# Kernel tuning notes

Hardware: AMD Instinct MI355X
Metric: run time of the kernel (lower is better)

Reference implementation:

```python
import jax, jax.numpy as jnp
import numpy as np

N_NODES = 50000
N_EDGES = 800000
IN_FEAT = 256
OUT_FEAT = 256
NUM_RELS = 64
NUM_BASES = 8


def setup_inputs() -> dict:
    key = jax.random.key(0)
    ks = jax.random.split(key, 9)
    x = jax.random.normal(ks[0], (N_NODES, IN_FEAT), dtype=jnp.float32)
    src = jax.random.randint(ks[1], (N_EDGES,), 0, N_NODES, dtype=jnp.int32)
    dst = jax.random.randint(ks[2], (N_EDGES,), 0, N_NODES, dtype=jnp.int32)
    etypes = jax.random.randint(ks[3], (N_EDGES,), 0, NUM_RELS, dtype=jnp.int32)
    norm = jax.random.uniform(ks[4], (N_EDGES, 1), dtype=jnp.float32)
    # glorot-style params
    s_w = (6.0 / (IN_FEAT + OUT_FEAT)) ** 0.5
    weight = jax.random.uniform(ks[5], (NUM_BASES, IN_FEAT, OUT_FEAT), jnp.float32, -s_w, s_w)
    s_c = (6.0 / (NUM_RELS + NUM_BASES)) ** 0.5
    w_comp = jax.random.uniform(ks[6], (NUM_RELS, NUM_BASES), jnp.float32, -s_c, s_c)
    h_bias = jnp.zeros((OUT_FEAT,), jnp.float32)
    loop_weight = jax.random.uniform(ks[7], (IN_FEAT, OUT_FEAT), jnp.float32, -s_w, s_w)
    return {"x": x, "src": src, "dst": dst, "etypes": etypes, "norm": norm,
            "weight": weight, "w_comp": w_comp, "h_bias": h_bias,
            "loop_weight": loop_weight}


def reference(x, src, dst, etypes, norm, weight, w_comp, h_bias, loop_weight):
    # Basis regularizer with num_bases < num_rels:
    #   W_r = sum_b w_comp[r, b] * V_b
    # Per-edge message: msg_e = (x[src_e] @ W_{etype_e}) * norm_e,
    # aggregated by sum onto destination nodes. Since the map is linear,
    # we aggregate per basis first, then apply V_b (8 dense GEMMs).
    n_nodes = x.shape[0]
    coef = w_comp[etypes]                      # [E, B] per-edge basis coeffs
    xs = x[src] * norm                         # [E, D] normalized source feats
    out = jnp.zeros((n_nodes, weight.shape[2]), x.dtype)
    for b in range(weight.shape[0]):           # small fixed loop over bases
        agg = jax.ops.segment_sum(xs * coef[:, b:b + 1], dst,
                                  num_segments=n_nodes)   # [N, D]
        out = out + agg @ weight[b]            # [N, O]
    out = out + h_bias + x @ loop_weight       # bias + self-loop
    return jax.nn.relu(out)
```

## Files before the change

### kernel.cpp

```cpp
#include <hip/hip_runtime.h>
#include <hip/hip_bf16.h>
#include <stdint.h>

#define N_NODES 50000
#define N_EDGES 800000
#define IN_FEAT 256
#define OUT_FEAT 256
#define NUM_RELS 64
#define NUM_BASES 8
#define KTOT 2304
#define KAGG 2048
#define MP 50176
#define NT 36
#define SCAN_BLKS 196

typedef __attribute__((ext_vector_type(8))) __bf16 bf16x8;
typedef __attribute__((ext_vector_type(4))) __bf16 bf16x4;
typedef __attribute__((ext_vector_type(4))) float f32x4;
typedef __attribute__((ext_vector_type(2))) float f32x2;

static __device__ __forceinline__ void gload_lds16(const void* g, void* l) {
  auto gp = (const __attribute__((address_space(1))) void*)(uintptr_t)g;
  auto lp = (__attribute__((address_space(3))) void*)(uint32_t)(uintptr_t)l;
  __builtin_amdgcn_global_load_lds(gp, lp, 16, 0, 0);
}

__global__ void k_prex(const float* __restrict__ x, __bf16* __restrict__ xb) {
  int i = blockIdx.x * 256 + threadIdx.x;
  const float4* xp = (const float4*)x;
  float4 u = xp[i * 2], v = xp[i * 2 + 1];
  bf16x8 o;
  o[0] = (__bf16)u.x; o[1] = (__bf16)u.y; o[2] = (__bf16)u.z; o[3] = (__bf16)u.w;
  o[4] = (__bf16)v.x; o[5] = (__bf16)v.y; o[6] = (__bf16)v.z; o[7] = (__bf16)v.w;
  *(bf16x8*)(xb + (size_t)i * 8) = o;
}

__global__ void k_count(const int* __restrict__ dst, int* __restrict__ deg) {
  int e = blockIdx.x * 256 + threadIdx.x;
  atomicAdd(&deg[dst[e]], 1);
}

__global__ void k_scan1(const int* __restrict__ deg, int* __restrict__ offs,
                        int* __restrict__ bsum) {
  __shared__ int s[256];
  int t = threadIdx.x;
  int i = blockIdx.x * 256 + t;
  int v = (i < N_NODES) ? deg[i] : 0;
  s[t] = v;
  __syncthreads();
  for (int d = 1; d < 256; d <<= 1) {
    int y = (t >= d) ? s[t - d] : 0;
    __syncthreads();
    s[t] += y;
    __syncthreads();
  }
  if (i < N_NODES) offs[i] = s[t] - v;
  if (t == 255) bsum[blockIdx.x] = s[255];
}

__global__ void k_scan3(int* __restrict__ offs, const int* __restrict__ bsum,
                        int* __restrict__ fill) {
  __shared__ int s[256];
  int t = threadIdx.x;
  s[t] = (t < SCAN_BLKS && t < blockIdx.x) ? bsum[t] : 0;
  __syncthreads();
  for (int d = 128; d; d >>= 1) {
    if (t < d) s[t] += s[t + d];
    __syncthreads();
  }
  int base = s[0];
  int i = blockIdx.x * 256 + t;
  if (i < N_NODES) {
    int o = offs[i] + base;
    offs[i] = o;
    fill[i] = o;
  }
}

__global__ void k_scatter(const int* __restrict__ dst, const int* __restrict__ srcv,
                          const int* __restrict__ ety, const float* __restrict__ norm,
                          int* __restrict__ fill, uint2* __restrict__ erec) {
  int e = blockIdx.x * 256 + threadIdx.x;
  int pos = atomicAdd(&fill[dst[e]], 1);
  erec[pos] = make_uint2((unsigned)srcv[e] | ((unsigned)ety[e] << 16),
                         __float_as_uint(norm[e]));
}

#define AGG_BODY(RX, RY, XV)                                                  \
  do {                                                                        \
    int et_ = (RX) >> 16;                                                     \
    float nm_ = __uint_as_float(RY);                                          \
    f32x2 v0_ = {__uint_as_float((XV).x << 16) * nm_,                         \
                 __uint_as_float((XV).x & 0xffff0000u) * nm_};                 \
    f32x2 v1_ = {__uint_as_float((XV).y << 16) * nm_,                         \
                 __uint_as_float((XV).y & 0xffff0000u) * nm_};                 \
    f32x4 cl_ = *(const f32x4*)&wc[et_ * 8];                                  \
    f32x4 ch_ = *(const f32x4*)&wc[et_ * 8 + 4];                              \
    _Pragma("unroll") for (int b = 0; b < 4; ++b) {                           \
      acc[b][0] += v0_ * cl_[b];                                              \
      acc[b][1] += v1_ * cl_[b];                                              \
      acc[b + 4][0] += v0_ * ch_[b];                                          \
      acc[b + 4][1] += v1_ * ch_[b];                                          \
    }                                                                         \
  } while (0)

__global__ __launch_bounds__(256) void k_agg(
    const __bf16* __restrict__ xb, const float* __restrict__ w_comp,
    const int* __restrict__ offs, const int* __restrict__ fin,
    const uint2* __restrict__ erec, __bf16* __restrict__ A) {
  __shared__ float wc[NUM_RELS * NUM_BASES];
  int t = threadIdx.x;
  wc[t] = w_comp[t];
  wc[t + 256] = w_comp[t + 256];
  __syncthreads();

  int wid = t >> 6, lane = t & 63;
  int node = blockIdx.x * 4 + wid;

  f32x2 acc[NUM_BASES][2];
#pragma unroll
  for (int b = 0; b < NUM_BASES; ++b) {
    acc[b][0] = f32x2{0.f, 0.f};
    acc[b][1] = f32x2{0.f, 0.f};
  }

  int i0 = offs[node];
  int cnt = fin[node] - i0;
  const uint2* rp = erec + i0;
  int lo4 = lane * 4;

  int i = 0;
  for (; i + 8 <= cnt; i += 8) {
    uint2 r[8];
#pragma unroll
    for (int j = 0; j < 8; ++j) r[j] = rp[i + j];
    uint2 xv[8];
#pragma unroll
    for (int j = 0; j < 8; ++j)
      xv[j] = *(const uint2*)(xb + (size_t)(r[j].x & 0xffff) * IN_FEAT + lo4);
#pragma unroll
    for (int j = 0; j < 8; ++j) AGG_BODY(r[j].x, r[j].y, xv[j]);
  }
  for (; i + 4 <= cnt; i += 4) {
    uint2 r[4];
#pragma unroll
    for (int j = 0; j < 4; ++j) r[j] = rp[i + j];
    uint2 xv[4];
#pragma unroll
    for (int j = 0; j < 4; ++j)
      xv[j] = *(const uint2*)(xb + (size_t)(r[j].x & 0xffff) * IN_FEAT + lo4);
#pragma unroll
    for (int j = 0; j < 4; ++j) AGG_BODY(r[j].x, r[j].y, xv[j]);
  }
  for (; i < cnt; ++i) {
    uint2 r = rp[i];
    uint2 xv = *(const uint2*)(xb + (size_t)(r.x & 0xffff) * IN_FEAT + lo4);
    AGG_BODY(r.x, r.y, xv);
  }

  __bf16* Ar = A + (size_t)node * KAGG + lo4;
#pragma unroll
  for (int b = 0; b < NUM_BASES; ++b) {
    bf16x4 o;
    o[0] = (__bf16)acc[b][0][0];
    o[1] = (__bf16)acc[b][0][1];
    o[2] = (__bf16)acc[b][1][0];
    o[3] = (__bf16)acc[b][1][1];
    *(bf16x4*)(Ar + b * 256) = o;
  }
}

__global__ void k_prepw(const float* __restrict__ weight, const float* __restrict__ loop_w,
                        __bf16* __restrict__ Wt) {
  int o = blockIdx.x;
  int t = threadIdx.x;
#pragma unroll
  for (int c = 0; c < 9; ++c) {
    int r = c * 256 + t;
    float v = (r < 2048) ? weight[(size_t)r * 256 + o]
                         : loop_w[(size_t)(r - 2048) * 256 + o];
    Wt[(size_t)o * KTOT + r] = (__bf16)v;
  }
}

__global__ __launch_bounds__(512, 1) void k_gemm(const __bf16* __restrict__ A,
                                                 const __bf16* __restrict__ xb,
                                                 const __bf16* __restrict__ Wt,
                                                 const float* __restrict__ bias,
                                                 float* __restrict__ out) {
  __shared__ __align__(16) __bf16 sA[2 * 256 * 64];
  __shared__ __align__(16) __bf16 sB[2 * 256 * 64];

  int t = threadIdx.x;
  int wid = t >> 6, lane = t & 63;
  int tm = blockIdx.x;
  int wr = wid >> 2;
  int wcol = wid & 3;
  int rfw = __builtin_amdgcn_readfirstlane(wid);

  f32x4 acc[8][4];
#pragma unroll
  for (int m = 0; m < 8; ++m)
#pragma unroll
    for (int n = 0; n < 4; ++n) acc[m][n] = f32x4{0.f, 0.f, 0.f, 0.f};

  int frow = lane & 15;
  int g = lane >> 4;
  int f7 = frow & 7;
  int kb0 = ((g ^ f7) << 4);
  int kb1 = (((4 + g) ^ f7) << 4);

  int rh = t >> 3;
  int qoff = ((t & 7) ^ (rh & 7)) * 8;
  const __bf16* gA[2][2];
  const __bf16* gX[2][2];
  const __bf16* gB[2][2];
#pragma unroll
  for (int h = 0; h < 2; ++h)
#pragma unroll
    for (int it = 0; it < 2; ++it) {
      int row = h * 128 + it * 64 + rh;
      gA[h][it] = A + (size_t)(tm * 256 + row) * KAGG + qoff;
      gX[h][it] = xb + (size_t)(tm * 256 + row) * IN_FEAT + qoff;
      gB[h][it] = Wt + (size_t)row * KTOT + qoff;
    }

  bf16x8 af[4][2];
  bf16x8 bh0[2][2], bh1[2][2];

#define VMWAIT(N) asm volatile("s_waitcnt vmcnt(" #N ")" ::: "memory")
#define BAR()                                       \
  do {                                              \
    asm volatile("" ::: "memory");                  \
    __builtin_amdgcn_s_barrier();                   \
    asm volatile("" ::: "memory");                  \
  } while (0)
#define PRIO(N) __builtin_amdgcn_s_setprio(N)

#define STAGE_A(H, U, BUF)                                                    \
  do {                                                                        \
    char* d_ = (char*)sA + (BUF) * 32768 + (H) * 16384 + rfw * 1024;          \
    if ((U) < 32) {                                                           \
      int ko_ = (U) * 64;                                                     \
      gload_lds16(gA[H][0] + ko_, d_);                                        \
      gload_lds16(gA[H][1] + ko_, d_ + 8192);                                 \
    } else {                                                                  \
      int ko_ = ((U) - 32) * 64;                                              \
      gload_lds16(gX[H][0] + ko_, d_);                                        \
      gload_lds16(gX[H][1] + ko_, d_ + 8192);                                 \
    }                                                                         \
  } while (0)

#define STAGE_B(H, U, BUF)                                                    \
  do {                                                                        \
    char* d_ = (char*)sB + (BUF) * 32768 + (H) * 16384 + rfw * 1024;          \
    int ko_ = (U) * 64;                                                       \
    gload_lds16(gB[H][0] + ko_, d_);                                          \
    gload_lds16(gB[H][1] + ko_, d_ + 8192);                                   \
  } while (0)

#define READ_A(BUF, MS)                                                       \
  do {                                                                        \
    const char* b_ = (const char*)sA + (BUF) * 32768;                         \
    _Pragma("unroll") for (int mf = 0; mf < 4; ++mf) {                        \
      int r_ = wr * 128 + (MS) * 64 + mf * 16 + frow;                         \
      af[mf][0] = *(const bf16x8*)(b_ + r_ * 128 + kb0);                      \
      af[mf][1] = *(const bf16x8*)(b_ + r_ * 128 + kb1);                      \
    }                                                                         \
  } while (0)

#define READ_B(BUF, NH, DST)                                                  \
  do {                                                                        \
    const char* b_ = (const char*)sB + (BUF) * 32768;                         \
    _Pragma("unroll") for (int nf = 0; nf < 2; ++nf) {                        \
      int r_ = wcol * 64 + ((NH) * 2 + nf) * 16 + frow;                       \
      DST[nf][0] = *(const bf16x8*)(b_ + r_ * 128 + kb0);                     \
      DST[nf][1] = *(const bf16x8*)(b_ + r_ * 128 + kb1);                     \
    }                                                                         \
  } while (0)

#define MFMA16(MS, NH, BS)                                                    \
  do {                                                                        \
    _Pragma("unroll") for (int mf = 0; mf < 4; ++mf)                          \
    _Pragma("unroll") for (int nf = 0; nf < 2; ++nf) {                        \
      acc[(MS) * 4 + mf][(NH) * 2 + nf] =                                     \
          __builtin_amdgcn_mfma_f32_16x16x32_bf16(                            \
              af[mf][0], BS[nf][0], acc[(MS) * 4 + mf][(NH) * 2 + nf], 0, 0, 0);\
      acc[(MS) * 4 + mf][(NH) * 2 + nf] =                                     \
          __builtin_amdgcn_mfma_f32_16x16x32_bf16(                            \
              af[mf][1], BS[nf][1], acc[(MS) * 4 + mf][(NH) * 2 + nf], 0, 0, 0);\
    }                                                                         \
  } while (0)

  STAGE_A(0, 0, 0);
  STAGE_A(1, 0, 0);
  STAGE_B(0, 0, 0);
  STAGE_B(1, 0, 0);
  STAGE_A(0, 1, 1);
  VMWAIT(2);
  BAR();

  for (int kt = 0; kt < NT; ++kt) {
    int cb = kt & 1, nb = cb ^ 1;
    int u1 = (kt + 1 < NT) ? kt + 1 : NT - 1;
    int u2 = (kt + 2 < NT) ? kt + 2 : NT - 1;
    READ_A(cb, 0);
    READ_B(cb, 0, bh0);
    STAGE_A(1, u1, nb);
    BAR(); PRIO(1); MFMA16(0, 0, bh0); PRIO(0); BAR();
    READ_B(cb, 1, bh1);
    STAGE_B(0, u1, nb);
    BAR(); PRIO(1); MFMA16(0, 1, bh1); PRIO(0); BAR();
    READ_A(cb, 1);
    STAGE_B(1, u1, nb);
    BAR(); PRIO(1); MFMA16(1, 0, bh0); PRIO(0); BAR();
    STAGE_A(0, u2, cb);
    BAR(); PRIO(1); MFMA16(1, 1, bh1); PRIO(0);
    VMWAIT(2);
    BAR();
  }
#undef STAGE_A
#undef STAGE_B
#undef READ_A
#undef READ_B
#undef MFMA16
#undef VMWAIT
#undef BAR
#undef PRIO

  int r0 = (lane >> 4) * 4;
  int c0 = lane & 15;
#pragma unroll
  for (int m = 0; m < 8; ++m) {
    int rowb = tm * 256 + wr * 128 + m * 16 + r0;
#pragma unroll
    for (int n = 0; n < 4; ++n) {
      int col = wcol * 64 + n * 16 + c0;
      float bv = bias[col];
#pragma unroll
      for (int r = 0; r < 4; ++r) {
        int row = rowb + r;
        if (row < N_NODES) {
          float v = acc[m][n][r] + bv;
          out[(size_t)row * OUT_FEAT + col] = v > 0.f ? v : 0.f;
        }
      }
    }
  }
}

extern "C" void kernel_launch(void* const* d_in, const int* in_sizes, int n_in,
                              void* d_out, int out_size, void* d_ws, size_t ws_size,
                              hipStream_t stream) {
  const float* x      = (const float*)d_in[0];
  const int*   src    = (const int*)d_in[1];
  const int*   dst    = (const int*)d_in[2];
  const int*   ety    = (const int*)d_in[3];
  const float* norm   = (const float*)d_in[4];
  const float* weight = (const float*)d_in[5];
  const float* w_comp = (const float*)d_in[6];
  const float* h_bias = (const float*)d_in[7];
  const float* loop_w = (const float*)d_in[8];
  float* out = (float*)d_out;

  char* ws = (char*)d_ws;
  __bf16* A  = (__bf16*)ws;
  size_t off = (size_t)MP * KAGG * 2;
  __bf16* xb = (__bf16*)(ws + off);
  off += (size_t)MP * IN_FEAT * 2;
  __bf16* Wt = (__bf16*)(ws + off);
  off += (size_t)256 * KTOT * 2;
  uint2* erec = (uint2*)(ws + off);
  off += (size_t)N_EDGES * 8;
  int* deg   = (int*)(ws + off);
  int* offs  = deg + N_NODES;
  int* fill  = offs + N_NODES;
  int* bsum  = fill + N_NODES;

  hipMemsetAsync(deg, 0, N_NODES * sizeof(int), stream);
  k_prex<<<(N_NODES * IN_FEAT / 8) / 256, 256, 0, stream>>>(x, xb);
  k_count<<<N_EDGES / 256, 256, 0, stream>>>(dst, deg);
  k_scan1<<<SCAN_BLKS, 256, 0, stream>>>(deg, offs, bsum);
  k_scan3<<<SCAN_BLKS, 256, 0, stream>>>(offs, bsum, fill);
  k_scatter<<<N_EDGES / 256, 256, 0, stream>>>(dst, src, ety, norm, fill, erec);
  k_agg<<<N_NODES / 4, 256, 0, stream>>>(xb, w_comp, offs, fill, erec, A);
  k_prepw<<<256, 256, 0, stream>>>(weight, loop_w, Wt);
  k_gemm<<<MP / 256, 512, 0, stream>>>(A, xb, Wt, h_bias, out);
}
```

Measured before the change: 294.3 us.

## Restructure GEMM to 64-row tiles with B fragments loaded directly from pre-swizzled weights

Weights are pre-packed into MFMA fragment order so each wave loads its B operands straight from global memory (cached in L2) into registers, with no LDS staging. The GEMM tile shrinks from 256x256 with 512 threads to 64x256 with 256 threads, uses a 3-buffer A pipeline, and allows two blocks per CU. This cuts LDS traffic and barrier count per k-step and gives more blocks for occupancy. In exchange, B is re-read from L2 by every block, and the A-to-B reuse per block is lower.

```diff
diff --git a/kernel.cpp b/kernel.cpp
--- a/kernel.cpp
+++ b/kernel.cpp
@@ -170,37 +170,41 @@
   }
 }
 
-__global__ void k_prepw(const float* __restrict__ weight, const float* __restrict__ loop_w,
-                        __bf16* __restrict__ Wt) {
-  int o = blockIdx.x;
-  int t = threadIdx.x;
-#pragma unroll
-  for (int c = 0; c < 9; ++c) {
-    int r = c * 256 + t;
-    float v = (r < 2048) ? weight[(size_t)r * 256 + o]
+__global__ void k_prepwf(const float* __restrict__ weight, const float* __restrict__ loop_w,
+                         __bf16* __restrict__ Wf) {
+  int tid = blockIdx.x * 256 + threadIdx.x;
+  int lane6 = tid & 63;
+  int F = tid >> 6;
+  int kt2 = F >> 4;
+  int nf = F & 15;
+  int o = nf * 16 + (lane6 & 15);
+  int rbase = kt2 * 32 + (lane6 >> 4) * 8;
+  bf16x8 v;
+#pragma unroll
+  for (int j = 0; j < 8; ++j) {
+    int r = rbase + j;
+    float f = (r < 2048) ? weight[(size_t)r * 256 + o]
                          : loop_w[(size_t)(r - 2048) * 256 + o];
-    Wt[(size_t)o * KTOT + r] = (__bf16)v;
-  }
-}
-
-__global__ __launch_bounds__(512, 1) void k_gemm(const __bf16* __restrict__ A,
+    v[j] = (__bf16)f;
+  }
+  *(bf16x8*)(Wf + (size_t)tid * 8) = v;
+}
+
+__global__ __launch_bounds__(256, 2) void k_gemm(const __bf16* __restrict__ A,
                                                  const __bf16* __restrict__ xb,
-                                                 const __bf16* __restrict__ Wt,
+                                                 const __bf16* __restrict__ Wf,
                                                  const float* __restrict__ bias,
                                                  float* __restrict__ out) {
-  __shared__ __align__(16) __bf16 sA[2 * 256 * 64];
-  __shared__ __align__(16) __bf16 sB[2 * 256 * 64];
+  __shared__ __align__(16) __bf16 sA[3 * 64 * 64];
 
   int t = threadIdx.x;
   int wid = t >> 6, lane = t & 63;
   int tm = blockIdx.x;
-  int wr = wid >> 2;
-  int wcol = wid & 3;
   int rfw = __builtin_amdgcn_readfirstlane(wid);
 
-  f32x4 acc[8][4];
-#pragma unroll
-  for (int m = 0; m < 8; ++m)
+  f32x4 acc[4][4];
+#pragma unroll
+  for (int m = 0; m < 4; ++m)
 #pragma unroll
     for (int n = 0; n < 4; ++n) acc[m][n] = f32x4{0.f, 0.f, 0.f, 0.f};
 
@@ -212,21 +216,17 @@
 
   int rh = t >> 3;
   int qoff = ((t & 7) ^ (rh & 7)) * 8;
-  const __bf16* gA[2][2];
-  const __bf16* gX[2][2];
-  const __bf16* gB[2][2];
-#pragma unroll
-  for (int h = 0; h < 2; ++h)
-#pragma unroll
-    for (int it = 0; it < 2; ++it) {
-      int row = h * 128 + it * 64 + rh;
-      gA[h][it] = A + (size_t)(tm * 256 + row) * KAGG + qoff;
-      gX[h][it] = xb + (size_t)(tm * 256 + row) * IN_FEAT + qoff;
-      gB[h][it] = Wt + (size_t)row * KTOT + qoff;
-    }
-
-  bf16x8 af[4][2];
-  bf16x8 bh0[2][2], bh1[2][2];
+  const __bf16* gA[2];
+  const __bf16* gX[2];
+#pragma unroll
+  for (int it = 0; it < 2; ++it) {
+    int row = it * 32 + rh;
+    gA[it] = A + (size_t)(tm * 64 + row) * KAGG + qoff;
+    gX[it] = xb + (size_t)(tm * 64 + row) * IN_FEAT + qoff;
+  }
+  const __bf16* wfb = Wf + (size_t)(wid * 4) * 512 + lane * 8;
+
+  bf16x8 af[4][2], bcur[4][2];
 
 #define VMWAIT(N) asm volatile("s_waitcnt vmcnt(" #N ")" ::: "memory")
 #define BAR()                                       \
@@ -235,107 +235,83 @@
     __builtin_amdgcn_s_barrier();                   \
     asm volatile("" ::: "memory");                  \
   } while (0)
-#define PRIO(N) __builtin_amdgcn_s_setprio(N)
-
-#define STAGE_A(H, U, BUF)                                                    \
-  do {                                                                        \
-    char* d_ = (char*)sA + (BUF) * 32768 + (H) * 16384 + rfw * 1024;          \
+
+#define STAGE(U, BUF)                                                         \
+  do {                                                                        \
+    char* d_ = (char*)sA + (BUF) * 8192;                                      \
     if ((U) < 32) {                                                           \
       int ko_ = (U) * 64;                                                     \
-      gload_lds16(gA[H][0] + ko_, d_);                                        \
-      gload_lds16(gA[H][1] + ko_, d_ + 8192);                                 \
+      gload_lds16(gA[0] + ko_, d_ + rfw * 1024);                              \
+      gload_lds16(gA[1] + ko_, d_ + 4096 + rfw * 1024);                       \
     } else {                                                                  \
       int ko_ = ((U) - 32) * 64;                                              \
-      gload_lds16(gX[H][0] + ko_, d_);                                        \
-      gload_lds16(gX[H][1] + ko_, d_ + 8192);                                 \
-    }                                                                         \
-  } while (0)
-
-#define STAGE_B(H, U, BUF)                                                    \
-  do {                                                                        \
-    char* d_ = (char*)sB + (BUF) * 32768 + (H) * 16384 + rfw * 1024;          \
-    int ko_ = (U) * 64;                                                       \
-    gload_lds16(gB[H][0] + ko_, d_);                                          \
-    gload_lds16(gB[H][1] + ko_, d_ + 8192);                                   \
-  } while (0)
-
-#define READ_A(BUF, MS)                                                       \
-  do {                                                                        \
-    const char* b_ = (const char*)sA + (BUF) * 32768;                         \
+      gload_lds16(gX[0] + ko_, d_ + rfw * 1024);                              \
+      gload_lds16(gX[1] + ko_, d_ + 4096 + rfw * 1024);                       \
+    }                                                                         \
+  } while (0)
+
+#define LOADB(KT)                                                             \
+  do {                                                                        \
+    _Pragma("unroll") for (int nf = 0; nf < 4; ++nf) {                        \
+      bcur[nf][0] = *(const bf16x8*)(wfb + (size_t)(((KT) * 2 + 0) * 16 + nf) * 512); \
+      bcur[nf][1] = *(const bf16x8*)(wfb + (size_t)(((KT) * 2 + 1) * 16 + nf) * 512); \
+    }                                                                         \
+  } while (0)
+
+#define READ_A(BUF)                                                           \
+  do {                                                                        \
+    const char* b_ = (const char*)sA + (BUF) * 8192;                          \
     _Pragma("unroll") for (int mf = 0; mf < 4; ++mf) {                        \
-      int r_ = wr * 128 + (MS) * 64 + mf * 16 + frow;                         \
+      int r_ = mf * 16 + frow;                                                \
       af[mf][0] = *(const bf16x8*)(b_ + r_ * 128 + kb0);                      \
       af[mf][1] = *(const bf16x8*)(b_ + r_ * 128 + kb1);                      \
     }                                                                         \
   } while (0)
 
-#define READ_B(BUF, NH, DST)                                                  \
-  do {                                                                        \
-    const char* b_ = (const char*)sB + (BUF) * 32768;                         \
-    _Pragma("unroll") for (int nf = 0; nf < 2; ++nf) {                        \
-      int r_ = wcol * 64 + ((NH) * 2 + nf) * 16 + frow;                       \
-      DST[nf][0] = *(const bf16x8*)(b_ + r_ * 128 + kb0);                     \
-      DST[nf][1] = *(const bf16x8*)(b_ + r_ * 128 + kb1);                     \
-    }                                                                         \
-  } while (0)
-
-#define MFMA16(MS, NH, BS)                                                    \
+#define MFMA32()                                                              \
   do {                                                                        \
     _Pragma("unroll") for (int mf = 0; mf < 4; ++mf)                          \
-    _Pragma("unroll") for (int nf = 0; nf < 2; ++nf) {                        \
-      acc[(MS) * 4 + mf][(NH) * 2 + nf] =                                     \
-          __builtin_amdgcn_mfma_f32_16x16x32_bf16(                            \
-              af[mf][0], BS[nf][0], acc[(MS) * 4 + mf][(NH) * 2 + nf], 0, 0, 0);\
-      acc[(MS) * 4 + mf][(NH) * 2 + nf] =                                     \
-          __builtin_amdgcn_mfma_f32_16x16x32_bf16(                            \
-              af[mf][1], BS[nf][1], acc[(MS) * 4 + mf][(NH) * 2 + nf], 0, 0, 0);\
-    }                                                                         \
-  } while (0)
-
-  STAGE_A(0, 0, 0);
-  STAGE_A(1, 0, 0);
-  STAGE_B(0, 0, 0);
-  STAGE_B(1, 0, 0);
-  STAGE_A(0, 1, 1);
+    _Pragma("unroll") for (int nf = 0; nf < 4; ++nf) {                        \
+      acc[mf][nf] = __builtin_amdgcn_mfma_f32_16x16x32_bf16(                  \
+          af[mf][0], bcur[nf][0], acc[mf][nf], 0, 0, 0);                      \
+      acc[mf][nf] = __builtin_amdgcn_mfma_f32_16x16x32_bf16(                  \
+          af[mf][1], bcur[nf][1], acc[mf][nf], 0, 0, 0);                      \
+    }                                                                         \
+  } while (0)
+
+  STAGE(0, 0);
+  STAGE(1, 1);
   VMWAIT(2);
   BAR();
 
   for (int kt = 0; kt < NT; ++kt) {
-    int cb = kt & 1, nb = cb ^ 1;
-    int u1 = (kt + 1 < NT) ? kt + 1 : NT - 1;
+    int cb = kt % 3;
+    int nb = (kt + 2) % 3;
     int u2 = (kt + 2 < NT) ? kt + 2 : NT - 1;
-    READ_A(cb, 0);
-    READ_B(cb, 0, bh0);
-    STAGE_A(1, u1, nb);
-    BAR(); PRIO(1); MFMA16(0, 0, bh0); PRIO(0); BAR();
-    READ_B(cb, 1, bh1);
-    STAGE_B(0, u1, nb);
-    BAR(); PRIO(1); MFMA16(0, 1, bh1); PRIO(0); BAR();
-    READ_A(cb, 1);
-    STAGE_B(1, u1, nb);
-    BAR(); PRIO(1); MFMA16(1, 0, bh0); PRIO(0); BAR();
-    STAGE_A(0, u2, cb);
-    BAR(); PRIO(1); MFMA16(1, 1, bh1); PRIO(0);
+    LOADB(kt);
+    STAGE(u2, nb);
+    READ_A(cb);
+    __builtin_amdgcn_s_setprio(1);
+    MFMA32();
+    __builtin_amdgcn_s_setprio(0);
     VMWAIT(2);
     BAR();
   }
-#undef STAGE_A
-#undef STAGE_B
+#undef STAGE
+#undef LOADB
 #undef READ_A
-#undef READ_B
-#undef MFMA16
+#undef MFMA32
 #undef VMWAIT
 #undef BAR
-#undef PRIO
 
   int r0 = (lane >> 4) * 4;
   int c0 = lane & 15;
 #pragma unroll
-  for (int m = 0; m < 8; ++m) {
-    int rowb = tm * 256 + wr * 128 + m * 16 + r0;
+  for (int m = 0; m < 4; ++m) {
+    int rowb = tm * 64 + m * 16 + r0;
 #pragma unroll
     for (int n = 0; n < 4; ++n) {
-      int col = wcol * 64 + n * 16 + c0;
+      int col = wid * 64 + n * 16 + c0;
       float bv = bias[col];
 #pragma unroll
       for (int r = 0; r < 4; ++r) {
@@ -368,7 +344,7 @@
   size_t off = (size_t)MP * KAGG * 2;
   __bf16* xb = (__bf16*)(ws + off);
   off += (size_t)MP * IN_FEAT * 2;
-  __bf16* Wt = (__bf16*)(ws + off);
+  __bf16* Wf = (__bf16*)(ws + off);
   off += (size_t)256 * KTOT * 2;
   uint2* erec = (uint2*)(ws + off);
   off += (size_t)N_EDGES * 8;
@@ -384,6 +360,6 @@
   k_scan3<<<SCAN_BLKS, 256, 0, stream>>>(offs, bsum, fill);
   k_scatter<<<N_EDGES / 256, 256, 0, stream>>>(dst, src, ety, norm, fill, erec);
   k_agg<<<N_NODES / 4, 256, 0, stream>>>(xb, w_comp, offs, fill, erec, A);
-  k_prepw<<<256, 256, 0, stream>>>(weight, loop_w, Wt);
-  k_gemm<<<MP / 256, 512, 0, stream>>>(A, xb, Wt, h_bias, out);
-}
+  k_prepwf<<<288, 256, 0, stream>>>(weight, loop_w, Wf);
+  k_gemm<<<MP / 64, 256, 0, stream>>>(A, xb, Wf, h_bias, out);
+}
```

After: 309.2 us. +5.1%, slower.
